# Kernel tuning notes

Measured on AMD Instinct MI355X. Metric: run time of the kernel, lower is better.

Reference implementation:

```python
import jax, jax.numpy as jnp
import numpy as np

MODEL_DIM = 128
N_FRAMES = 128
N_SAMPLES = 32768
N_TABLES = 8
TABLE_SIZE = 512
BATCH = 8
N_FREQS = 16


def _mlp(x, w1, b1, w2, b2, w3, b3):
    # LinearOutputStack(channels, 3, ...): Linear -> lrelu -> Linear -> lrelu -> Linear
    h = jax.nn.leaky_relu(x @ w1 + b1, 0.2)
    h = jax.nn.leaky_relu(h @ w2 + b2, 0.2)
    return h @ w3 + b3


def _pos_encoded(t, n_freqs=N_FREQS):
    # (t, 1 + 2*n_freqs) = (t, 33): raw position plus sin/cos at geometric freqs
    pos = jnp.linspace(-1.0, 1.0, t, dtype=jnp.float32)
    scales = (2.0 ** jnp.arange(n_freqs, dtype=jnp.float32)) * jnp.pi
    ang = pos[:, None] * scales[None, :]
    return jnp.concatenate([pos[:, None], jnp.sin(ang), jnp.cos(ang)], axis=-1)


def _interp_linear(env, out_size):
    # torch F.interpolate(mode='linear', align_corners=False) from (B, F) to (B, out_size)
    f = env.shape[-1]
    coord = (jnp.arange(out_size, dtype=jnp.float32) + 0.5) * (f / out_size) - 0.5
    i0 = jnp.floor(coord)
    frac = (coord - i0).astype(env.dtype)
    i0c = jnp.clip(i0, 0, f - 1).astype(jnp.int32)
    i1c = jnp.clip(i0 + 1, 0, f - 1).astype(jnp.int32)
    return env[:, i0c] * (1.0 - frac) + env[:, i1c] * frac


def setup_inputs() -> dict:
    key = jax.random.key(0)
    ks = jax.random.split(key, 16)
    wi = 0.02  # weight_init from Experiment
    d = MODEL_DIM

    def lin(k, i, o):
        return jax.random.normal(k, (i, o), jnp.float32) * wi

    inp = {
        "x": jax.random.normal(ks[0], (BATCH, d), jnp.float32),
        "wavetables": jax.random.uniform(ks[1], (N_TABLES, TABLE_SIZE), jnp.float32, -1.0, 1.0),
    }
    specs = {"tc": (d, N_TABLES), "env": (d, N_FRAMES), "pos": (33, d), "sk": (d, TABLE_SIZE)}
    i = 2
    for name, (cin, cout) in specs.items():
        k1, k2, k3 = jax.random.split(ks[i], 3)
        inp[f"{name}_w1"] = lin(k1, cin, d)
        inp[f"{name}_b1"] = jnp.zeros((d,), jnp.float32)
        inp[f"{name}_w2"] = lin(k2, d, d)
        inp[f"{name}_b2"] = jnp.zeros((d,), jnp.float32)
        inp[f"{name}_w3"] = lin(k3, d, cout)
        inp[f"{name}_b3"] = jnp.zeros((cout,), jnp.float32)
        i += 1
    return inp


def reference(x, wavetables,
              tc_w1, tc_b1, tc_w2, tc_b2, tc_w3, tc_b3,
              env_w1, env_b1, env_w2, env_b2, env_w3, env_b3,
              pos_w1, pos_b1, pos_w2, pos_b2, pos_w3, pos_b3,
              sk_w1, sk_b1, sk_w2, sk_b2, sk_w3, sk_b3):
    # table choice: softmax then hard max (straight value * gathered table)
    c = jax.nn.softmax(_mlp(x, tc_w1, tc_b1, tc_w2, tc_b2, tc_w3, tc_b3), axis=-1)
    values = jnp.max(c, axis=-1)          # (B,)
    indices = jnp.argmax(c, axis=-1)      # (B,)

    mx = jnp.max(wavetables, axis=-1, keepdims=True)
    wt = wavetables / (mx + 1e-8)
    sel = wt[indices]                     # (B, TABLE_SIZE)

    env = jnp.abs(_mlp(x, env_w1, env_b1, env_w2, env_b2, env_w3, env_b3))  # (B, N_FRAMES)
    env = _interp_linear(env, N_SAMPLES)  # (B, N_SAMPLES)

    # pos encoding is identical across batch; embed once then broadcast (same math)
    pe = _pos_encoded(N_SAMPLES)          # (T, 33)
    pos = _mlp(pe, pos_w1, pos_b1, pos_w2, pos_b2, pos_w3, pos_b3)  # (T, D)
    pos = pos[None, :, :] + x[:, None, :]  # (B, T, D)

    sk = jax.nn.softmax(_mlp(pos, sk_w1, sk_b1, sk_w2, sk_b2, sk_w3, sk_b3), axis=-1)  # (B, T, K)

    # selected_tables (B,1,K) @ kernel^T (B,K,T) -> (B,1,T)
    sampled = jnp.einsum('bk,btk->bt', sel, sk)
    sampled = sampled * env * values[:, None]
    return sampled[:, None, :]
```

## Files before the change

kernel.cpp:

```cpp
#include <hip/hip_runtime.h>
#include <math.h>

#define D 128
#define B 8
#define T_SAMP 32768
#define K 512
#define NT 8
#define NFRM 128

#define WS_C1   0
#define WS_ENV8 1024
#define WS_SEL  2048
#define WS_VAL  6144
#define WSBF_BYTE 32768
#define OP1 0
#define OP2 9216
#define OP3 26624
#define OS1 44032
#define OS2 61440
#define OS3 78848
#define WTOT 148480
#define WS_NEED (WSBF_BYTE + WTOT*2)

typedef __attribute__((ext_vector_type(8))) short short8;
typedef __attribute__((ext_vector_type(4))) float f32x4;

__device__ __forceinline__ float lrelu(float v){ return v >= 0.0f ? v : 0.2f*v; }

__device__ __forceinline__ unsigned pk2(float lo, float hi){
    unsigned a = __builtin_bit_cast(unsigned, lo); a += 0x7fffu + ((a>>16)&1u);
    unsigned b = __builtin_bit_cast(unsigned, hi); b += 0x7fffu + ((b>>16)&1u);
    return (a>>16) | (b & 0xffff0000u);
}
__device__ __forceinline__ unsigned short bfr(float f){
    unsigned u = __builtin_bit_cast(unsigned, f); u += 0x7fffu + ((u>>16)&1u);
    return (unsigned short)(u>>16);
}
__device__ __forceinline__ float bf2f(short s){
    unsigned u = ((unsigned)(unsigned short)s) << 16;
    return __builtin_bit_cast(float, u);
}

#define VMCNT0 asm volatile("s_waitcnt vmcnt(0)" ::: "memory")

__device__ void layer128(const float* __restrict__ in, const float* __restrict__ w,
                         const float* __restrict__ bias, float* __restrict__ outp,
                         int tid, int mode)
{
    int n = tid & 127, bg = tid >> 7;
    const float* i0 = in + (bg*4+0)*D;
    const float* i1 = in + (bg*4+1)*D;
    const float* i2 = in + (bg*4+2)*D;
    const float* i3 = in + (bg*4+3)*D;
    float bb = bias[n];
    float a0=bb,a1=bb,a2=bb,a3=bb;
    for (int j=0;j<D;j++){
        float wv = w[j*D+n];
        a0 = fmaf(i0[j], wv, a0);
        a1 = fmaf(i1[j], wv, a1);
        a2 = fmaf(i2[j], wv, a2);
        a3 = fmaf(i3[j], wv, a3);
    }
    if (mode==0){ a0=lrelu(a0);a1=lrelu(a1);a2=lrelu(a2);a3=lrelu(a3); }
    else if (mode==1){ a0=fabsf(a0);a1=fabsf(a1);a2=fabsf(a2);a3=fabsf(a3); }
    outp[(bg*4+0)*D+n]=a0;
    outp[(bg*4+1)*D+n]=a1;
    outp[(bg*4+2)*D+n]=a2;
    outp[(bg*4+3)*D+n]=a3;
}

__global__ __launch_bounds__(256) void setup_kernel(
    const float* __restrict__ x, const float* __restrict__ wt,
    const float* __restrict__ tc_w1, const float* __restrict__ tc_b1,
    const float* __restrict__ tc_w2, const float* __restrict__ tc_b2,
    const float* __restrict__ tc_w3, const float* __restrict__ tc_b3,
    const float* __restrict__ env_w1, const float* __restrict__ env_b1,
    const float* __restrict__ env_w2, const float* __restrict__ env_b2,
    const float* __restrict__ env_w3, const float* __restrict__ env_b3,
    const float* __restrict__ sk_w1, const float* __restrict__ sk_b1,
    const float* __restrict__ pos_w1, const float* __restrict__ pos_w2,
    const float* __restrict__ pos_w3, const float* __restrict__ sk_w2,
    const float* __restrict__ sk_w3,
    float* __restrict__ ws)
{
    __shared__ float xl[B*D], buf1[B*D], buf2[B*D];
    __shared__ float lgts[B*NT], pmax[NT*8], mxr[NT];
    __shared__ int idxl[B];
    int tid = threadIdx.x;

    if (blockIdx.x != 0){
        int idx = (blockIdx.x - 1)*256 + tid;
        if (idx >= WTOT) return;
        unsigned short* wb = (unsigned short*)((char*)ws + WSBF_BYTE);
        float v;
        if (idx < OP2){
            int n = idx/72, k = idx%72;
            v = (k < 33) ? pos_w1[k*D + n] : 0.f;
        } else if (idx < OS3){
            int r = idx - OP2; int wsel = r/17408; int i = r%17408;
            int n = i/136, k = i%136;
            const float* W = wsel==0?pos_w2: wsel==1?pos_w3: wsel==2? sk_w1 : sk_w2;
            v = (k < 128) ? W[k*D + n] : 0.f;
        } else {
            int i = idx - OS3; int n = i/136, k = i%136;
            v = (k < 128) ? sk_w3[k*K + n] : 0.f;
        }
        wb[idx] = bfr(v);
        return;
    }

    for (int i=tid;i<B*D;i+=256) xl[i]=x[i];
    __syncthreads();
    layer128(xl, tc_w1, tc_b1, buf1, tid, 0);
    __syncthreads();
    layer128(buf1, tc_w2, tc_b2, buf2, tid, 0);
    __syncthreads();
    if (tid < 64){
        int b = tid>>3, n = tid&7;
        float a = tc_b3[n];
        for (int j=0;j<D;j++) a = fmaf(buf2[b*D+j], tc_w3[j*NT+n], a);
        lgts[b*NT+n] = a;
    } else if (tid < 128){
        int r = (tid-64)>>3, p = tid&7;
        float m = -1e30f;
        for (int k=p*64;k<p*64+64;k++) m = fmaxf(m, wt[r*K+k]);
        pmax[r*8+p] = m;
    }
    __syncthreads();
    if (tid < 8){
        int b = tid; float m = -1e30f; int idx = 0;
        for (int n=0;n<NT;n++){ float v = lgts[b*NT+n]; if (v > m){ m=v; idx=n; } }
        float S = 0.f;
        for (int n=0;n<NT;n++) S += expf(lgts[b*NT+n]-m);
        ws[WS_VAL+b] = 1.0f/S;
        idxl[b] = idx;
    } else if (tid < 16){
        int r = tid-8; float m = -1e30f;
        for (int p=0;p<8;p++) m = fmaxf(m, pmax[r*8+p]);
        mxr[r] = m;
    }
    __syncthreads();
    for (int o=tid;o<B*K;o+=256){
        int b = o>>9, k = o&(K-1);
        int id = idxl[b];
        ws[WS_SEL+o] = wt[id*K+k] / (mxr[id] + 1e-8f);
    }
    layer128(xl, env_w1, env_b1, buf1, tid, 0);
    __syncthreads();
    layer128(buf1, env_w2, env_b2, buf2, tid, 0);
    __syncthreads();
    layer128(buf2, env_w3, env_b3, ws+WS_ENV8, tid, 1);
    layer128(xl, sk_w1, sk_b1, ws+WS_C1, tid, 2);
}

__global__ __launch_bounds__(512, 4) void synth3(
    const float* __restrict__ pos_b1, const float* __restrict__ pos_b2,
    const float* __restrict__ pos_b3, const float* __restrict__ sk_b2,
    const float* __restrict__ sk_b3,
    const float* __restrict__ ws, float* __restrict__ out)
{
    __shared__ __align__(16) unsigned char lds[77184];
    unsigned char* WREG_ = lds;
    unsigned char* abA   = lds + 34816;
    unsigned char* abB   = lds + 43520;
    unsigned char* PEb   = abB;
    float* C1f  = (float*)(lds + 52224);
    float* BIAf = (float*)(lds + 56448);
    float* SELf = (float*)(lds + 60544);

    const int tid = threadIdx.x;
    const int wv = tid >> 6, lane = tid & 63, lg = lane >> 4, lc = lane & 15;
    const int t0 = blockIdx.x * 32;
    const unsigned char* wg = (const unsigned char*)ws + WSBF_BYTE;
    const f32x4 z = {0.f,0.f,0.f,0.f};

    auto stage = [&](int elemoff, unsigned char* dst, int nchunks){
        const unsigned char* src = wg + (size_t)elemoff*2;
        for (int c = wv; c < nchunks; c += 8)
            __builtin_amdgcn_global_load_lds(
                (const __attribute__((address_space(1))) unsigned int*)(src + (c<<10) + lane*16),
                (__attribute__((address_space(3))) unsigned int*)(dst + (c<<10)), 16, 0, 0);
    };

    stage(OP1, WREG_, 18);
    for (int i = tid; i < 1152; i += 512){
        int r = i/36, pj = i - r*36;
        int j0 = pj*2;
        float v[2];
        #pragma unroll
        for (int u=0; u<2; u++){
            int j = j0 + u;
            float pf = (float)(-1.0 + 2.0*(double)(t0+r)/32767.0);
            float vv = 0.f;
            if (j == 0) vv = pf;
            else if (j <= 16) vv = sinf(pf * ((float)M_PI * (float)(1<<(j-1))));
            else if (j <= 32) vv = cosf(pf * ((float)M_PI * (float)(1<<(j-17))));
            v[u] = vv;
        }
        *(unsigned*)(PEb + (r*72 + j0)*2) = pk2(v[0], v[1]);
    }
    for (int i=tid;i<1024;i+=512) C1f[(i>>7)*132 + (i&127)] = ws[WS_C1+i];
    for (int i=tid;i<1024;i+=512){
        float v;
        if (i<128) v = pos_b1[i]; else if (i<256) v = pos_b2[i-128];
        else if (i<384) v = pos_b3[i-256]; else if (i<512) v = sk_b2[i-384];
        else v = sk_b3[i-512];
        BIAf[i] = v;
    }
    for (int i=tid;i<4096;i+=512) SELf[(i>>9)*520 + (i&511)] = ws[WS_SEL+i];
    VMCNT0; __syncthreads();

    auto layerG = [&](const unsigned char* Wp, int kstride, int nkt,
                      const unsigned char* inb, int instride,
                      unsigned char* outb, int biaso, int act){
        short8 aw[4];
        for (int kt=0;kt<nkt;kt++)
            aw[kt] = *(const short8*)(Wp + ((16*wv+lc)*kstride + 32*kt + 8*lg)*2);
        f32x4 bb = z;
        if (biaso >= 0) bb = *(const f32x4*)(BIAf + biaso + 16*wv + 4*lg);
        for (int rt=0;rt<2;rt++){
            f32x4 d = z;
            for (int kt=0;kt<nkt;kt++){
                short8 bf = *(const short8*)(inb + ((16*rt+lc)*instride + 32*kt + 8*lg)*2);
                d = __builtin_amdgcn_mfma_f32_16x16x32_bf16(aw[kt], bf, d, 0,0,0);
            }
            float o[4];
            #pragma unroll
            for (int q=0;q<4;q++){
                float vv = d[q] + bb[q];
                o[q] = act ? lrelu(vv) : vv;
            }
            uint2 u; u.x = pk2(o[0],o[1]); u.y = pk2(o[2],o[3]);
            *(uint2*)(outb + ((16*rt+lc)*136 + 16*wv + 4*lg)*2) = u;
        }
    };

    layerG(WREG_, 72, 2, PEb, 72, abA, 0, 1);
    __syncthreads();
    stage(OP2, WREG_, 34); VMCNT0; __syncthreads();
    layerG(WREG_, 136, 4, abA, 136, abB, 128, 1);
    __syncthreads();
    stage(OP3, WREG_, 34); VMCNT0; __syncthreads();
    layerG(WREG_, 136, 4, abB, 136, abA, 256, 0);
    __syncthreads();
    stage(OS1, WREG_, 34); VMCNT0; __syncthreads();
    layerG(WREG_, 136, 4, abA, 136, abB, -1, 0);
    __syncthreads();

    stage(OS2, WREG_, 34);
    short8 hf[2][4];
    {
        const int b = lc & 7;
        #pragma unroll
        for (int rtl=0;rtl<2;rtl++){
            int tl = 4*wv + 2*rtl + (lc>>3);
            #pragma unroll
            for (int kt=0;kt<4;kt++){
                short8 a1v = *(const short8*)(abB + (tl*136 + 32*kt + 8*lg)*2);
                const float* cp = C1f + b*132 + 32*kt + 8*lg;
                f32x4 c0 = *(const f32x4*)cp;
                f32x4 c1v = *(const f32x4*)(cp+4);
                float h[8];
                #pragma unroll
                for (int e=0;e<4;e++) h[e]   = lrelu(bf2f(a1v[e])   + c0[e]);
                #pragma unroll
                for (int e=0;e<4;e++) h[4+e] = lrelu(bf2f(a1v[4+e]) + c1v[e]);
                uint4 t4; t4.x=pk2(h[0],h[1]); t4.y=pk2(h[2],h[3]);
                t4.z=pk2(h[4],h[5]); t4.w=pk2(h[6],h[7]);
                hf[rtl][kt] = __builtin_bit_cast(short8, t4);
            }
        }
    }
    VMCNT0; __syncthreads();

    short8 h2B[2][4];
    {
        const int sA = (2*(lg&1))*16 + lc;
        const int sB = sA + 16;
        const bool hi = (lg>>1) != 0;
        #pragma unroll
        for (int kt2=0; kt2<4; kt2++){
            unsigned dpk[2][2][2];
            #pragma unroll
            for (int p=0;p<2;p++){
                int n2t = 2*kt2+p;
                short8 aw[4];
                #pragma unroll
                for (int kt=0;kt<4;kt++)
                    aw[kt] = *(const short8*)(WREG_ + ((16*n2t+lc)*136 + 32*kt + 8*lg)*2);
                f32x4 b2 = *(const f32x4*)(BIAf + 384 + 16*n2t + 4*lg);
                #pragma unroll
                for (int rtl=0;rtl<2;rtl++){
                    f32x4 d = z;
                    #pragma unroll
                    for (int kt=0;kt<4;kt++)
                        d = __builtin_amdgcn_mfma_f32_16x16x32_bf16(aw[kt], hf[rtl][kt], d, 0,0,0);
                    float o[4];
                    #pragma unroll
                    for (int q=0;q<4;q++) o[q] = lrelu(d[q] + b2[q]);
                    dpk[p][rtl][0] = pk2(o[0],o[1]);
                    dpk[p][rtl][1] = pk2(o[2],o[3]);
                }
            }
            #pragma unroll
            for (int rtl=0;rtl<2;rtl++){
                unsigned a0 = (unsigned)__shfl((int)dpk[0][rtl][0], sA, 64);
                unsigned b0 = (unsigned)__shfl((int)dpk[1][rtl][0], sA, 64);
                unsigned a1 = (unsigned)__shfl((int)dpk[0][rtl][1], sA, 64);
                unsigned b1 = (unsigned)__shfl((int)dpk[1][rtl][1], sA, 64);
                unsigned a2 = (unsigned)__shfl((int)dpk[0][rtl][0], sB, 64);
                unsigned b2u= (unsigned)__shfl((int)dpk[1][rtl][0], sB, 64);
                unsigned a3 = (unsigned)__shfl((int)dpk[0][rtl][1], sB, 64);
                unsigned b3u= (unsigned)__shfl((int)dpk[1][rtl][1], sB, 64);
                uint4 uu;
                uu.x = hi ? b0 : a0;  uu.y = hi ? b1 : a1;
                uu.z = hi ? b2u : a2; uu.w = hi ? b3u : a3;
                h2B[rtl][kt2] = __builtin_bit_cast(short8, uu);
            }
        }
    }
    __syncthreads();

    float SSa[2][4], WWa[2][4];
    #pragma unroll
    for (int r=0;r<2;r++)
        #pragma unroll
        for (int q=0;q<4;q++){ SSa[r][q]=0.f; WWa[r][q]=0.f; }

    stage(OS3, WREG_, 17); VMCNT0; __syncthreads();
    const int selb = (lc & 7)*520;
    for (int c=0;c<8;c++){
        const unsigned char* slot = WREG_ + (c&1)*17408;
        if (c < 7) stage(OS3 + (c+1)*8704, WREG_ + ((c+1)&1)*17408, 17);
        #pragma unroll
        for (int nl=0;nl<4;nl++){
            int n3t = 4*c + nl;
            short8 bw[4];
            #pragma unroll
            for (int kt=0;kt<4;kt++)
                bw[kt] = *(const short8*)(slot + ((16*nl+lc)*136 + 32*kt + 8*lg)*2);
            f32x4 d3[2]; d3[0]=z; d3[1]=z;
            #pragma unroll
            for (int rtl=0;rtl<2;rtl++){
                #pragma unroll
                for (int kt=0;kt<4;kt++)
                    d3[rtl] = __builtin_amdgcn_mfma_f32_16x16x32_bf16(bw[kt], h2B[rtl][kt], d3[rtl], 0,0,0);
            }
            f32x4 b3 = *(const f32x4*)(BIAf + 512 + 16*n3t + 4*lg);
            f32x4 sv = *(const f32x4*)(SELf + selb + 16*n3t + 4*lg);
            #pragma unroll
            for (int rtl=0;rtl<2;rtl++){
                #pragma unroll
                for (int q=0;q<4;q++){
                    float e = __expf(d3[rtl][q] + b3[q]);
                    SSa[rtl][q] += e;
                    WWa[rtl][q] = fmaf(e, sv[q], WWa[rtl][q]);
                }
            }
        }
        VMCNT0; __syncthreads();
    }

    #pragma unroll
    for (int rtl=0;rtl<2;rtl++){
        float s = SSa[rtl][0]+SSa[rtl][1]+SSa[rtl][2]+SSa[rtl][3];
        float w = WWa[rtl][0]+WWa[rtl][1]+WWa[rtl][2]+WWa[rtl][3];
        s += __shfl_xor(s, 16, 64); s += __shfl_xor(s, 32, 64);
        w += __shfl_xor(w, 16, 64); w += __shfl_xor(w, 32, 64);
        if (lg == 0){
            int tl = 4*wv + 2*rtl + (lc>>3);
            int b  = lc & 7;
            int t  = t0 + tl;
            float coord = (t + 0.5f)*(1.0f/256.0f) - 0.5f;
            float fi = floorf(coord); float frac = coord - fi;
            int i0 = (int)fi; int i1 = i0 + 1;
            i0 = min(max(i0,0),NFRM-1); i1 = min(max(i1,0),NFRM-1);
            float e0 = ws[WS_ENV8 + b*NFRM + i0], e1 = ws[WS_ENV8 + b*NFRM + i1];
            float envv = e0*(1.0f-frac) + e1*frac;
            out[b*T_SAMP + t] = (w/s) * envv * ws[WS_VAL+b];
        }
    }
}

extern "C" void kernel_launch(void* const* d_in, const int* in_sizes, int n_in,
                              void* d_out, int out_size, void* d_ws, size_t ws_size,
                              hipStream_t stream)
{
    (void)in_sizes; (void)n_in; (void)out_size;
    const float* x       = (const float*)d_in[0];
    const float* wt      = (const float*)d_in[1];
    const float* tc_w1   = (const float*)d_in[2];
    const float* tc_b1   = (const float*)d_in[3];
    const float* tc_w2   = (const float*)d_in[4];
    const float* tc_b2   = (const float*)d_in[5];
    const float* tc_w3   = (const float*)d_in[6];
    const float* tc_b3   = (const float*)d_in[7];
    const float* env_w1  = (const float*)d_in[8];
    const float* env_b1  = (const float*)d_in[9];
    const float* env_w2  = (const float*)d_in[10];
    const float* env_b2  = (const float*)d_in[11];
    const float* env_w3  = (const float*)d_in[12];
    const float* env_b3  = (const float*)d_in[13];
    const float* pos_w1  = (const float*)d_in[14];
    const float* pos_b1  = (const float*)d_in[15];
    const float* pos_w2  = (const float*)d_in[16];
    const float* pos_b2  = (const float*)d_in[17];
    const float* pos_w3  = (const float*)d_in[18];
    const float* pos_b3  = (const float*)d_in[19];
    const float* sk_w1   = (const float*)d_in[20];
    const float* sk_b1   = (const float*)d_in[21];
    const float* sk_w2   = (const float*)d_in[22];
    const float* sk_b2   = (const float*)d_in[23];
    const float* sk_w3   = (const float*)d_in[24];
    const float* sk_b3   = (const float*)d_in[25];
    float* ws  = (float*)d_ws;
    float* out = (float*)d_out;

    if (ws_size < (size_t)WS_NEED) return;

    hipLaunchKernelGGL(setup_kernel, dim3(1 + (WTOT+255)/256), dim3(256), 0, stream,
        x, wt, tc_w1, tc_b1, tc_w2, tc_b2, tc_w3, tc_b3,
        env_w1, env_b1, env_w2, env_b2, env_w3, env_b3,
        sk_w1, sk_b1, pos_w1, pos_w2, pos_w3, sk_w2, sk_w3, ws);

    hipLaunchKernelGGL(synth3, dim3(T_SAMP/32), dim3(512), 0, stream,
        pos_b1, pos_b2, pos_b3, sk_b2, sk_b3, ws, out);
}
```

Before: 104.2 us.

## Shrink LDS footprint, use hardware bf16 pack, exp2 and revolution-based sin/cos

Moves the C1, bias and selected-table arrays out of LDS and reads them from global memory instead. This cuts shared memory from about 77KB to about 52KB, and the launch bound is raised to request more resident blocks. It also swaps the software bf16 rounding for v_cvt_pk_bf16_f32 and turns the lambda layer into a templated function. The softmax exp becomes exp2 with log2e folded into a prescaled sk_b3, and the positional-encoding sin/cos use the hardware revolution-based instructions. The trade-off is extra global or cached loads in the hot loop in exchange for occupancy and fewer ALU instructions, plus small accuracy differences in the PE and exp paths.

```diff
diff --git a/kernel.cpp b/kernel.cpp
--- a/kernel.cpp
+++ b/kernel.cpp
@@ -12,6 +12,7 @@
 #define WS_ENV8 1024
 #define WS_SEL  2048
 #define WS_VAL  6144
+#define WS_B3P  6160
 #define WSBF_BYTE 32768
 #define OP1 0
 #define OP2 9216
@@ -25,12 +26,14 @@
 typedef __attribute__((ext_vector_type(8))) short short8;
 typedef __attribute__((ext_vector_type(4))) float f32x4;
 
-__device__ __forceinline__ float lrelu(float v){ return v >= 0.0f ? v : 0.2f*v; }
-
-__device__ __forceinline__ unsigned pk2(float lo, float hi){
-    unsigned a = __builtin_bit_cast(unsigned, lo); a += 0x7fffu + ((a>>16)&1u);
-    unsigned b = __builtin_bit_cast(unsigned, hi); b += 0x7fffu + ((b>>16)&1u);
-    return (a>>16) | (b & 0xffff0000u);
+#define LOG2E 1.4426950408889634f
+
+__device__ __forceinline__ float lrelu(float v){ return fmaxf(v, 0.2f*v); }
+
+__device__ __forceinline__ unsigned cvtpk(float lo, float hi){
+    unsigned r;
+    asm("v_cvt_pk_bf16_f32 %0, %1, %2" : "=v"(r) : "v"(lo), "v"(hi));
+    return r;
 }
 __device__ __forceinline__ unsigned short bfr(float f){
     unsigned u = __builtin_bit_cast(unsigned, f); u += 0x7fffu + ((u>>16)&1u);
@@ -39,6 +42,37 @@
 __device__ __forceinline__ float bf2f(short s){
     unsigned u = ((unsigned)(unsigned short)s) << 16;
     return __builtin_bit_cast(float, u);
+}
+__device__ __forceinline__ float exp2fast(float x){
+#if __has_builtin(__builtin_amdgcn_exp2f)
+    return __builtin_amdgcn_exp2f(x);
+#else
+    return __expf(x*0.6931471805599453f);
+#endif
+}
+__device__ __forceinline__ float sin_rev(float fr){
+#if __has_builtin(__builtin_amdgcn_sinf)
+    return __builtin_amdgcn_sinf(fr);
+#else
+    return __sinf(fr*6.283185307179586f);
+#endif
+}
+__device__ __forceinline__ float cos_rev(float fr){
+#if __has_builtin(__builtin_amdgcn_cosf)
+    return __builtin_amdgcn_cosf(fr);
+#else
+    return __cosf(fr*6.283185307179586f);
+#endif
+}
+__device__ __forceinline__ float pe_val(float pf, int j){
+    if (j == 0) return pf;
+    if (j > 32) return 0.f;
+    const bool is_sin = (j <= 16);
+    int e = is_sin ? (j + 125) : (j + 109);
+    float sc = __builtin_bit_cast(float, ((unsigned)e) << 23);
+    float u = pf * sc;
+    float fr = u - floorf(u);
+    return is_sin ? sin_rev(fr) : cos_rev(fr);
 }
 
 #define VMCNT0 asm volatile("s_waitcnt vmcnt(0)" ::: "memory")
@@ -80,7 +114,7 @@
     const float* __restrict__ sk_w1, const float* __restrict__ sk_b1,
     const float* __restrict__ pos_w1, const float* __restrict__ pos_w2,
     const float* __restrict__ pos_w3, const float* __restrict__ sk_w2,
-    const float* __restrict__ sk_w3,
+    const float* __restrict__ sk_w3, const float* __restrict__ sk_b3,
     float* __restrict__ ws)
 {
     __shared__ float xl[B*D], buf1[B*D], buf2[B*D];
@@ -110,6 +144,7 @@
     }
 
     for (int i=tid;i<B*D;i+=256) xl[i]=x[i];
+    for (int i=tid;i<K;i+=256) ws[WS_B3P+i] = sk_b3[i]*LOG2E;
     __syncthreads();
     layer128(xl, tc_w1, tc_b1, buf1, tid, 0);
     __syncthreads();
@@ -153,20 +188,43 @@
     layer128(xl, sk_w1, sk_b1, ws+WS_C1, tid, 2);
 }
 
-__global__ __launch_bounds__(512, 4) void synth3(
+template<int NKT, int KSTR, bool ACT>
+__device__ __forceinline__ void layerG(const unsigned char* Wp, const unsigned char* inb,
+                                       unsigned char* outb, const float* biasp,
+                                       int wv, int lg, int lc)
+{
+    const f32x4 z = {0.f,0.f,0.f,0.f};
+    short8 aw[NKT];
+    #pragma unroll
+    for (int kt=0;kt<NKT;kt++)
+        aw[kt] = *(const short8*)(Wp + ((16*wv+lc)*KSTR + 32*kt + 8*lg)*2);
+    f32x4 bb = z;
+    if (biasp) bb = *(const f32x4*)(biasp + 16*wv + 4*lg);
+    #pragma unroll
+    for (int rt=0;rt<2;rt++){
+        f32x4 d = z;
+        #pragma unroll
+        for (int kt=0;kt<NKT;kt++){
+            short8 bf = *(const short8*)(inb + ((16*rt+lc)*KSTR + 32*kt + 8*lg)*2);
+            d = __builtin_amdgcn_mfma_f32_16x16x32_bf16(aw[kt], bf, d, 0,0,0);
+        }
+        float o0 = d[0]+bb[0], o1 = d[1]+bb[1], o2 = d[2]+bb[2], o3 = d[3]+bb[3];
+        if (ACT){ o0=lrelu(o0); o1=lrelu(o1); o2=lrelu(o2); o3=lrelu(o3); }
+        uint2 u; u.x = cvtpk(o0,o1); u.y = cvtpk(o2,o3);
+        *(uint2*)(outb + ((16*rt+lc)*136 + 16*wv + 4*lg)*2) = u;
+    }
+}
+
+__global__ __launch_bounds__(512, 6) void synth3(
     const float* __restrict__ pos_b1, const float* __restrict__ pos_b2,
     const float* __restrict__ pos_b3, const float* __restrict__ sk_b2,
-    const float* __restrict__ sk_b3,
     const float* __restrict__ ws, float* __restrict__ out)
 {
-    __shared__ __align__(16) unsigned char lds[77184];
+    __shared__ __align__(16) unsigned char lds[52224];
     unsigned char* WREG_ = lds;
     unsigned char* abA   = lds + 34816;
     unsigned char* abB   = lds + 43520;
     unsigned char* PEb   = abB;
-    float* C1f  = (float*)(lds + 52224);
-    float* BIAf = (float*)(lds + 56448);
-    float* SELf = (float*)(lds + 60544);
 
     const int tid = threadIdx.x;
     const int wv = tid >> 6, lane = tid & 63, lg = lane >> 4, lc = lane & 15;
@@ -184,89 +242,48 @@
 
     stage(OP1, WREG_, 18);
     for (int i = tid; i < 1152; i += 512){
-        int r = i/36, pj = i - r*36;
-        int j0 = pj*2;
-        float v[2];
-        #pragma unroll
-        for (int u=0; u<2; u++){
-            int j = j0 + u;
-            float pf = (float)(-1.0 + 2.0*(double)(t0+r)/32767.0);
-            float vv = 0.f;
-            if (j == 0) vv = pf;
-            else if (j <= 16) vv = sinf(pf * ((float)M_PI * (float)(1<<(j-1))));
-            else if (j <= 32) vv = cosf(pf * ((float)M_PI * (float)(1<<(j-17))));
-            v[u] = vv;
-        }
-        *(unsigned*)(PEb + (r*72 + j0)*2) = pk2(v[0], v[1]);
-    }
-    for (int i=tid;i<1024;i+=512) C1f[(i>>7)*132 + (i&127)] = ws[WS_C1+i];
-    for (int i=tid;i<1024;i+=512){
-        float v;
-        if (i<128) v = pos_b1[i]; else if (i<256) v = pos_b2[i-128];
-        else if (i<384) v = pos_b3[i-256]; else if (i<512) v = sk_b2[i-384];
-        else v = sk_b3[i-512];
-        BIAf[i] = v;
-    }
-    for (int i=tid;i<4096;i+=512) SELf[(i>>9)*520 + (i&511)] = ws[WS_SEL+i];
+        int r = i/36, j0 = (i - r*36)*2;
+        float pf = (float)(-1.0 + 2.0*(double)(t0+r)/32767.0);
+        float v0 = pe_val(pf, j0);
+        float v1 = pe_val(pf, j0+1);
+        *(unsigned*)(PEb + (r*72 + j0)*2) = cvtpk(v0, v1);
+    }
     VMCNT0; __syncthreads();
 
-    auto layerG = [&](const unsigned char* Wp, int kstride, int nkt,
-                      const unsigned char* inb, int instride,
-                      unsigned char* outb, int biaso, int act){
-        short8 aw[4];
-        for (int kt=0;kt<nkt;kt++)
-            aw[kt] = *(const short8*)(Wp + ((16*wv+lc)*kstride + 32*kt + 8*lg)*2);
-        f32x4 bb = z;
-        if (biaso >= 0) bb = *(const f32x4*)(BIAf + biaso + 16*wv + 4*lg);
-        for (int rt=0;rt<2;rt++){
-            f32x4 d = z;
-            for (int kt=0;kt<nkt;kt++){
-                short8 bf = *(const short8*)(inb + ((16*rt+lc)*instride + 32*kt + 8*lg)*2);
-                d = __builtin_amdgcn_mfma_f32_16x16x32_bf16(aw[kt], bf, d, 0,0,0);
-            }
-            float o[4];
-            #pragma unroll
-            for (int q=0;q<4;q++){
-                float vv = d[q] + bb[q];
-                o[q] = act ? lrelu(vv) : vv;
-            }
-            uint2 u; u.x = pk2(o[0],o[1]); u.y = pk2(o[2],o[3]);
-            *(uint2*)(outb + ((16*rt+lc)*136 + 16*wv + 4*lg)*2) = u;
-        }
-    };
-
-    layerG(WREG_, 72, 2, PEb, 72, abA, 0, 1);
+    layerG<2,72,true>(WREG_, PEb, abA, pos_b1, wv, lg, lc);
     __syncthreads();
     stage(OP2, WREG_, 34); VMCNT0; __syncthreads();
-    layerG(WREG_, 136, 4, abA, 136, abB, 128, 1);
+    layerG<4,136,true>(WREG_, abA, abB, pos_b2, wv, lg, lc);
     __syncthreads();
     stage(OP3, WREG_, 34); VMCNT0; __syncthreads();
-    layerG(WREG_, 136, 4, abB, 136, abA, 256, 0);
+    layerG<4,136,false>(WREG_, abB, abA, pos_b3, wv, lg, lc);
     __syncthreads();
     stage(OS1, WREG_, 34); VMCNT0; __syncthreads();
-    layerG(WREG_, 136, 4, abA, 136, abB, -1, 0);
+    layerG<4,136,false>(WREG_, abA, abB, nullptr, wv, lg, lc);
     __syncthreads();
 
     stage(OS2, WREG_, 34);
     short8 hf[2][4];
     {
         const int b = lc & 7;
+        const float* c1g = ws + WS_C1 + b*128;
         #pragma unroll
         for (int rtl=0;rtl<2;rtl++){
             int tl = 4*wv + 2*rtl + (lc>>3);
             #pragma unroll
             for (int kt=0;kt<4;kt++){
                 short8 a1v = *(const short8*)(abB + (tl*136 + 32*kt + 8*lg)*2);
-                const float* cp = C1f + b*132 + 32*kt + 8*lg;
+                const float* cp = c1g + 32*kt + 8*lg;
                 f32x4 c0 = *(const f32x4*)cp;
                 f32x4 c1v = *(const f32x4*)(cp+4);
                 float h[8];
                 #pragma unroll
-                for (int e=0;e<4;e++) h[e]   = lrelu(bf2f(a1v[e])   + c0[e]);
-                #pragma unroll
-                for (int e=0;e<4;e++) h[4+e] = lrelu(bf2f(a1v[4+e]) + c1v[e]);
-                uint4 t4; t4.x=pk2(h[0],h[1]); t4.y=pk2(h[2],h[3]);
-                t4.z=pk2(h[4],h[5]); t4.w=pk2(h[6],h[7]);
+                for (int e=0;e<4;e++){
+                    h[e]   = lrelu(bf2f(a1v[e])   + c0[e]);
+                    h[4+e] = lrelu(bf2f(a1v[4+e]) + c1v[e]);
+                }
+                uint4 t4; t4.x=cvtpk(h[0],h[1]); t4.y=cvtpk(h[2],h[3]);
+                t4.z=cvtpk(h[4],h[5]); t4.w=cvtpk(h[6],h[7]);
                 hf[rtl][kt] = __builtin_bit_cast(short8, t4);
             }
         }
@@ -288,18 +305,17 @@
                 #pragma unroll
                 for (int kt=0;kt<4;kt++)
                     aw[kt] = *(const short8*)(WREG_ + ((16*n2t+lc)*136 + 32*kt + 8*lg)*2);
-                f32x4 b2 = *(const f32x4*)(BIAf + 384 + 16*n2t + 4*lg);
+                f32x4 b2 = *(const f32x4*)(sk_b2 + 16*n2t + 4*lg);
                 #pragma unroll
                 for (int rtl=0;rtl<2;rtl++){
                     f32x4 d = z;
                     #pragma unroll
                     for (int kt=0;kt<4;kt++)
                         d = __builtin_amdgcn_mfma_f32_16x16x32_bf16(aw[kt], hf[rtl][kt], d, 0,0,0);
-                    float o[4];
-                    #pragma unroll
-                    for (int q=0;q<4;q++) o[q] = lrelu(d[q] + b2[q]);
-                    dpk[p][rtl][0] = pk2(o[0],o[1]);
-                    dpk[p][rtl][1] = pk2(o[2],o[3]);
+                    float o0=lrelu(d[0]+b2[0]), o1=lrelu(d[1]+b2[1]);
+                    float o2=lrelu(d[2]+b2[2]), o3=lrelu(d[3]+b2[3]);
+                    dpk[p][rtl][0] = cvtpk(o0,o1);
+                    dpk[p][rtl][1] = cvtpk(o2,o3);
                 }
             }
             #pragma unroll
@@ -328,7 +344,8 @@
         for (int q=0;q<4;q++){ SSa[r][q]=0.f; WWa[r][q]=0.f; }
 
     stage(OS3, WREG_, 17); VMCNT0; __syncthreads();
-    const int selb = (lc & 7)*520;
+    const float* selg = ws + WS_SEL + (lc & 7)*512;
+    const float* b3g  = ws + WS_B3P;
     for (int c=0;c<8;c++){
         const unsigned char* slot = WREG_ + (c&1)*17408;
         if (c < 7) stage(OS3 + (c+1)*8704, WREG_ + ((c+1)&1)*17408, 17);
@@ -346,13 +363,13 @@
                 for (int kt=0;kt<4;kt++)
                     d3[rtl] = __builtin_amdgcn_mfma_f32_16x16x32_bf16(bw[kt], h2B[rtl][kt], d3[rtl], 0,0,0);
             }
-            f32x4 b3 = *(const f32x4*)(BIAf + 512 + 16*n3t + 4*lg);
-            f32x4 sv = *(const f32x4*)(SELf + selb + 16*n3t + 4*lg);
+            f32x4 b3 = *(const f32x4*)(b3g + 16*n3t + 4*lg);
+            f32x4 sv = *(const f32x4*)(selg + 16*n3t + 4*lg);
             #pragma unroll
             for (int rtl=0;rtl<2;rtl++){
                 #pragma unroll
                 for (int q=0;q<4;q++){
-                    float e = __expf(d3[rtl][q] + b3[q]);
+                    float e = exp2fast(fmaf(d3[rtl][q], LOG2E, b3[q]));
                     SSa[rtl][q] += e;
                     WWa[rtl][q] = fmaf(e, sv[q], WWa[rtl][q]);
                 }
@@ -421,8 +438,8 @@
     hipLaunchKernelGGL(setup_kernel, dim3(1 + (WTOT+255)/256), dim3(256), 0, stream,
         x, wt, tc_w1, tc_b1, tc_w2, tc_b2, tc_w3, tc_b3,
         env_w1, env_b1, env_w2, env_b2, env_w3, env_b3,
-        sk_w1, sk_b1, pos_w1, pos_w2, pos_w3, sk_w2, sk_w3, ws);
+        sk_w1, sk_b1, pos_w1, pos_w2, pos_w3, sk_w2, sk_w3, sk_b3, ws);
 
     hipLaunchKernelGGL(synth3, dim3(T_SAMP/32), dim3(512), 0, stream,
-        pos_b1, pos_b2, pos_b3, sk_b2, sk_b3, ws, out);
-}
+        pos_b1, pos_b2, pos_b3, sk_b2, ws, out);
+}
```

Measured after the change: 247.5 us. 2.38x slower.
